# Optimization experiments

Hardware: AMD Instinct MI355X
Metric: run time of the kernel (lower is better)

The kernel has to match this reference:

```python
import jax, jax.numpy as jnp
import numpy as np

N_NODES = 50000
N_EDGES = 800000
HIDDEN = 128
N_LAYERS = 3
EPS = 1e-5


def setup_inputs() -> dict:
    key = jax.random.key(0)
    ks = jax.random.split(key, 6)
    x = jax.random.normal(ks[0], (N_NODES, HIDDEN), dtype=jnp.float32)
    edge_index = jax.random.randint(ks[1], (2, N_EDGES), 0, N_NODES, dtype=jnp.int64)
    scale = 1.0 / np.sqrt(HIDDEN)
    Wl = jax.random.normal(ks[2], (N_LAYERS, HIDDEN, HIDDEN), dtype=jnp.float32) * scale
    bl = jnp.zeros((N_LAYERS, HIDDEN), dtype=jnp.float32)
    Wr = jax.random.normal(ks[3], (N_LAYERS, HIDDEN, HIDDEN), dtype=jnp.float32) * scale
    gamma = jnp.ones((N_LAYERS, HIDDEN), dtype=jnp.float32)
    beta = jnp.zeros((N_LAYERS, HIDDEN), dtype=jnp.float32)
    return {"x": x, "edge_index": edge_index, "Wl": Wl, "bl": bl,
            "Wr": Wr, "gamma": gamma, "beta": beta}


def reference(x, edge_index, Wl, bl, Wr, gamma, beta):
    # SAGEConv (mean aggr): out_i = Wl @ mean_{j in N(i)} x_j + bl + Wr @ x_i
    # followed by BatchNorm (batch stats), ReLU, residual (layers > 0).
    src, dst = edge_index[0], edge_index[1]
    N = x.shape[0]
    deg = jax.ops.segment_sum(jnp.ones((src.shape[0],), dtype=x.dtype), dst,
                              num_segments=N)
    inv_deg = (1.0 / jnp.maximum(deg, 1.0))[:, None]  # [N,1]; empty nbhd -> 0 agg
    for i in range(N_LAYERS):
        msg = x[src]                                            # [E,H] gather
        agg = jax.ops.segment_sum(msg, dst, num_segments=N) * inv_deg  # [N,H]
        h = agg @ Wl[i].T + bl[i] + x @ Wr[i].T                 # [N,H]
        mean = jnp.mean(h, axis=0)
        var = jnp.var(h, axis=0)                                # biased, as torch BN
        h = gamma[i] * (h - mean) * jax.lax.rsqrt(var + EPS) + beta[i]
        h = jax.nn.relu(h)
        x = h + x if i > 0 else h
    return x
```

## Files before the change

kernel.cpp:

```cpp
#include <hip/hip_runtime.h>

#define HH 128
#define EPS 1e-5f
#define NBMAX 256
#define SCAP 40
#define FCAP 12288

typedef __bf16 bf16x8 __attribute__((ext_vector_type(8)));
typedef float f32x4 __attribute__((ext_vector_type(4)));
typedef float f32x2 __attribute__((ext_vector_type(2)));

__device__ __forceinline__ unsigned f2bf(float f) {
    unsigned u = __builtin_bit_cast(unsigned, f);
    return (u + 0x7FFFu + ((u >> 16) & 1u)) >> 16;
}
__device__ __forceinline__ float bflo(unsigned w) { return __builtin_bit_cast(float, w << 16); }
__device__ __forceinline__ float bfhi(unsigned w) { return __builtin_bit_cast(float, w & 0xFFFF0000u); }

__device__ __forceinline__ unsigned pack_fp8x4(float f0, float f1, float f2, float f3) {
    unsigned r = 0;
    r = __builtin_amdgcn_cvt_pk_fp8_f32(f0, f1, r, false);
    r = __builtin_amdgcn_cvt_pk_fp8_f32(f2, f3, r, true);
    return r;
}

__device__ __forceinline__ void gload_lds16(const void* g, void* l) {
    __builtin_amdgcn_global_load_lds(
        (const __attribute__((address_space(1))) unsigned int*)g,
        (__attribute__((address_space(3))) unsigned int*)l,
        16, 0, 0);
}

__global__ __launch_bounds__(256) void convert_hist_kernel(
    const float* __restrict__ x, const float* __restrict__ Wl, const float* __restrict__ Wr,
    const int* __restrict__ dst,
    ushort* __restrict__ xb, unsigned* __restrict__ xq, ushort* __restrict__ Wb,
    int* __restrict__ bcnt,
    int n4, int m4, int wtotal, int E)
{
    __shared__ int h[NBMAX];
    const int t = threadIdx.x;
    h[t] = 0;
    __syncthreads();
    const int gt = blockIdx.x * 256 + t;
    const int gs = gridDim.x * 256;
    for (int e = gt; e < E; e += gs) atomicAdd(&h[dst[e] >> 8], 1);
    for (int i = gt; i < wtotal; i += gs) {
        int l = i / (HH * 256);
        int rem = i - l * (HH * 256);
        int col = rem >> 8;
        int k = rem & 255;
        float v = (k < HH) ? Wl[(size_t)l * HH * HH + col * HH + k]
                           : Wr[(size_t)l * HH * HH + col * HH + (k - HH)];
        Wb[i] = (ushort)f2bf(v);
    }
    for (int i = gt; i < m4; i += gs) {
        uint2 o = make_uint2(0u, 0u);
        unsigned q = 0u;
        if (i < n4) {
            float4 v = ((const float4*)x)[i];
            o.x = f2bf(v.x) | (f2bf(v.y) << 16);
            o.y = f2bf(v.z) | (f2bf(v.w) << 16);
            q = pack_fp8x4(v.x, v.y, v.z, v.w);
        }
        ((uint2*)xb)[i] = o;
        xq[i] = q;
    }
    __syncthreads();
    if (h[t]) atomicAdd(&bcnt[t], h[t]);
}

__global__ __launch_bounds__(256) void bucket_scan_kernel(const int* __restrict__ bcnt,
                                                          int* __restrict__ boff,
                                                          int* __restrict__ gpos, int NB, int E) {
    __shared__ int s[NBMAX];
    const int t = threadIdx.x;
    s[t] = (t < NB) ? bcnt[t] : 0;
    __syncthreads();
    for (int off = 1; off < 256; off <<= 1) {
        int u = (t >= off) ? s[t - off] : 0;
        __syncthreads();
        s[t] += u;
        __syncthreads();
    }
    int excl = (t == 0) ? 0 : s[t - 1];
    if (t < NB) { boff[t] = excl; gpos[t] = excl; }
    if (t == 0) boff[NB] = E;
}

__global__ __launch_bounds__(256) void bucket_scatter_kernel(
    const int* __restrict__ src, const int* __restrict__ dst,
    int* __restrict__ gpos, unsigned* __restrict__ packed, int E, int GRID)
{
    __shared__ unsigned q[NBMAX][SCAP];
    __shared__ int qc[NBMAX];
    const int t = threadIdx.x;
    const int b = blockIdx.x;
    qc[t] = 0;
    __syncthreads();
    const int ebeg = (int)((long)b * E / GRID);
    const int eend = (int)((long)(b + 1) * E / GRID);
    for (int base = ebeg; base < eend; base += 256) {
        int e = base + t;
        if (e < eend) {
            int d = dst[e];
            unsigned pk = ((unsigned)d << 16) | (unsigned)src[e];
            int bk = d >> 8;
            int slot = atomicAdd(&qc[bk], 1);
            if (slot < SCAP) q[bk][slot] = pk;
            else { int p = atomicAdd(&gpos[bk], 1); packed[p] = pk; }
        }
        __syncthreads();
        int c = qc[t]; if (c > SCAP) c = SCAP;
        if (c >= 32) {
            int p = atomicAdd(&gpos[t], 32);
            for (int i = 0; i < 32; ++i) packed[p + i] = q[t][i];
            for (int i = 32; i < c; ++i) q[t][i - 32] = q[t][i];
            qc[t] = c - 32;
        } else {
            qc[t] = c;
        }
        __syncthreads();
    }
    int c = qc[t]; if (c > SCAP) c = SCAP;
    if (c > 0) {
        int p = atomicAdd(&gpos[t], c);
        for (int i = 0; i < c; ++i) packed[p + i] = q[t][i];
    }
}

__global__ __launch_bounds__(256) void bucket_finalize_kernel(
    const unsigned* __restrict__ packed, const int* __restrict__ boff,
    int* __restrict__ row_ptr, float* __restrict__ invdeg,
    ushort* __restrict__ edge_csr, int N, int E)
{
    __shared__ int hist[256];
    __shared__ int posq[256];
    __shared__ ushort outq[FCAP];
    const int b = blockIdx.x, t = threadIdx.x;
    const int beg = boff[b], end = boff[b + 1], n = end - beg;
    hist[t] = 0;
    __syncthreads();
    for (int i = beg + t; i < end; i += 256)
        atomicAdd(&hist[(packed[i] >> 16) & 255], 1);
    __syncthreads();
    const int c = hist[t];
    for (int off = 1; off < 256; off <<= 1) {
        int u = (t >= off) ? hist[t - off] : 0;
        __syncthreads();
        hist[t] += u;
        __syncthreads();
    }
    const int excl = hist[t] - c;
    const int node = (b << 8) + t;
    if (node < N) {
        row_ptr[node] = beg + excl;
        invdeg[node] = 1.0f / fmaxf((float)c, 1.0f);
    }
    if (b == 0 && t == 0) row_ptr[N] = E;
    posq[t] = excl;
    __syncthreads();
    if (n <= FCAP) {
        for (int i = beg + t; i < end; i += 256) {
            unsigned pk = packed[i];
            int p = atomicAdd(&posq[(pk >> 16) & 255], 1);
            outq[p] = (ushort)(pk & 0xFFFFu);
        }
        __syncthreads();
        for (int i = t; i < n; i += 256) edge_csr[beg + i] = outq[i];
    } else {
        for (int i = beg + t; i < end; i += 256) {
            unsigned pk = packed[i];
            int p = atomicAdd(&posq[(pk >> 16) & 255], 1);
            edge_csr[beg + p] = (ushort)(pk & 0xFFFFu);
        }
    }
}

__global__ __launch_bounds__(256) void gather_kernel(
    const unsigned* __restrict__ xq, const int* __restrict__ row_ptr,
    const ushort* __restrict__ edge_csr, const float* __restrict__ invdeg,
    ushort* __restrict__ aggb, int N)
{
    const int node = blockIdx.x * 16 + (threadIdx.x >> 4);
    const int l16 = threadIdx.x & 15;
    float a0=0,a1=0,a2=0,a3=0,a4=0,a5=0,a6=0,a7=0;
    float id = 0.f;
    if (node < N) {
        const int beg = row_ptr[node], end = row_ptr[node + 1];
        id = invdeg[node];
        int e = beg;
        for (; e + 3 < end; e += 4) {
            int s0 = edge_csr[e], s1 = edge_csr[e + 1];
            int s2 = edge_csr[e + 2], s3 = edge_csr[e + 3];
            uint2 v0 = *(const uint2*)(xq + (size_t)s0 * 32 + l16 * 2);
            uint2 v1 = *(const uint2*)(xq + (size_t)s1 * 32 + l16 * 2);
            uint2 v2 = *(const uint2*)(xq + (size_t)s2 * 32 + l16 * 2);
            uint2 v3 = *(const uint2*)(xq + (size_t)s3 * 32 + l16 * 2);
            f32x2 p;
            p = __builtin_amdgcn_cvt_pk_f32_fp8(v0.x, false); a0 += p.x; a1 += p.y;
            p = __builtin_amdgcn_cvt_pk_f32_fp8(v0.x, true);  a2 += p.x; a3 += p.y;
            p = __builtin_amdgcn_cvt_pk_f32_fp8(v0.y, false); a4 += p.x; a5 += p.y;
            p = __builtin_amdgcn_cvt_pk_f32_fp8(v0.y, true);  a6 += p.x; a7 += p.y;
            p = __builtin_amdgcn_cvt_pk_f32_fp8(v1.x, false); a0 += p.x; a1 += p.y;
            p = __builtin_amdgcn_cvt_pk_f32_fp8(v1.x, true);  a2 += p.x; a3 += p.y;
            p = __builtin_amdgcn_cvt_pk_f32_fp8(v1.y, false); a4 += p.x; a5 += p.y;
            p = __builtin_amdgcn_cvt_pk_f32_fp8(v1.y, true);  a6 += p.x; a7 += p.y;
            p = __builtin_amdgcn_cvt_pk_f32_fp8(v2.x, false); a0 += p.x; a1 += p.y;
            p = __builtin_amdgcn_cvt_pk_f32_fp8(v2.x, true);  a2 += p.x; a3 += p.y;
            p = __builtin_amdgcn_cvt_pk_f32_fp8(v2.y, false); a4 += p.x; a5 += p.y;
            p = __builtin_amdgcn_cvt_pk_f32_fp8(v2.y, true);  a6 += p.x; a7 += p.y;
            p = __builtin_amdgcn_cvt_pk_f32_fp8(v3.x, false); a0 += p.x; a1 += p.y;
            p = __builtin_amdgcn_cvt_pk_f32_fp8(v3.x, true);  a2 += p.x; a3 += p.y;
            p = __builtin_amdgcn_cvt_pk_f32_fp8(v3.y, false); a4 += p.x; a5 += p.y;
            p = __builtin_amdgcn_cvt_pk_f32_fp8(v3.y, true);  a6 += p.x; a7 += p.y;
        }
        for (; e < end; ++e) {
            int s0 = edge_csr[e];
            uint2 v0 = *(const uint2*)(xq + (size_t)s0 * 32 + l16 * 2);
            f32x2 p;
            p = __builtin_amdgcn_cvt_pk_f32_fp8(v0.x, false); a0 += p.x; a1 += p.y;
            p = __builtin_amdgcn_cvt_pk_f32_fp8(v0.x, true);  a2 += p.x; a3 += p.y;
            p = __builtin_amdgcn_cvt_pk_f32_fp8(v0.y, false); a4 += p.x; a5 += p.y;
            p = __builtin_amdgcn_cvt_pk_f32_fp8(v0.y, true);  a6 += p.x; a7 += p.y;
        }
    }
    uint4 o;
    o.x = f2bf(a0 * id) | (f2bf(a1 * id) << 16);
    o.y = f2bf(a2 * id) | (f2bf(a3 * id) << 16);
    o.z = f2bf(a4 * id) | (f2bf(a5 * id) << 16);
    o.w = f2bf(a6 * id) | (f2bf(a7 * id) << 16);
    *(uint4*)(aggb + (size_t)node * HH + l16 * 8) = o;
}

__global__ __launch_bounds__(512) void fused_layer_kernel(
    const ushort* __restrict__ aggb, ushort* __restrict__ xb,
    const ushort* __restrict__ Wb, const float* __restrict__ bl,
    const float* __restrict__ gamma, const float* __restrict__ beta,
    float* __restrict__ stats, unsigned* __restrict__ bar,
    unsigned* __restrict__ xq, float* __restrict__ outf,
    float invN, int nblocks, int N, int residual, int final_layer)
{
    extern __shared__ ushort As[];
    __shared__ float s_sum[128];
    __shared__ float s_sum2[128];

    const int tid = threadIdx.x;
    const int lane = tid & 63;
    const int wave = tid >> 6;
    const int m0 = blockIdx.x * 256;
    const int l15 = lane & 15;
    const int lg = lane >> 4;
    const int col = wave * 16 + l15;

#pragma unroll
    for (int i = 0; i < 16; ++i) {
        const int cb = (i * 8 + wave) * 64;
        const int L = cb + lane;
        const int r = L >> 5;
        const int c = L & 31;
        const int cs = (c & 0x18) | ((c & 7) ^ (r & 7));
        const ushort* gsrc = (cs < 16)
            ? (aggb + (size_t)(m0 + r) * HH + cs * 8)
            : (xb   + (size_t)(m0 + r) * HH + (cs - 16) * 8);
        gload_lds16(gsrc, &As[(size_t)cb * 8]);
    }

    bf16x8 bfr[8];
#pragma unroll
    for (int s = 0; s < 8; ++s)
        bfr[s] = *(const bf16x8*)(Wb + (size_t)col * 256 + s * 32 + lg * 8);

    if (tid < 128) { s_sum[tid] = 0.f; s_sum2[tid] = 0.f; }

    f32x4 acc[16];
#pragma unroll
    for (int rt = 0; rt < 16; ++rt) acc[rt] = (f32x4){0.f, 0.f, 0.f, 0.f};

    __syncthreads();

#pragma unroll
    for (int s = 0; s < 8; ++s) {
#pragma unroll
        for (int rt = 0; rt < 16; ++rt) {
            const int r = rt * 16 + l15;
            const int g = s * 4 + lg;
            const int c = (g & 0x18) | ((g & 7) ^ (r & 7));
            bf16x8 a = *(const bf16x8*)&As[r * 256 + c * 8];
            acc[rt] = __builtin_amdgcn_mfma_f32_16x16x32_bf16(a, bfr[s], acc[rt], 0, 0, 0);
        }
    }

    const float bias = bl[col];
    float s1 = 0.f, s2 = 0.f;
#pragma unroll
    for (int rt = 0; rt < 16; ++rt) {
#pragma unroll
        for (int r = 0; r < 4; ++r) {
            const int row = rt * 16 + lg * 4 + r;
            if (m0 + row < N) {
                float v = acc[rt][r] + bias;
                s1 += v; s2 += v * v;
            }
        }
    }
    atomicAdd(&s_sum[col], s1);
    atomicAdd(&s_sum2[col], s2);
    __syncthreads();
    if (tid < 128) {
        atomicAdd(&stats[tid], s_sum[tid]);
        atomicAdd(&stats[128 + tid], s_sum2[tid]);
    }
    __syncthreads();
    if (tid == 0) {
        __hip_atomic_fetch_add(bar, 1u, __ATOMIC_ACQ_REL, __HIP_MEMORY_SCOPE_AGENT);
        while (__hip_atomic_load(bar, __ATOMIC_ACQUIRE, __HIP_MEMORY_SCOPE_AGENT) < (unsigned)nblocks)
            __builtin_amdgcn_s_sleep(8);
    }
    __syncthreads();

    const float sA = __hip_atomic_load(&stats[col], __ATOMIC_RELAXED, __HIP_MEMORY_SCOPE_AGENT);
    const float sB = __hip_atomic_load(&stats[128 + col], __ATOMIC_RELAXED, __HIP_MEMORY_SCOPE_AGENT);
    const float mean = sA * invN;
    const float var = sB * invN - mean * mean;
    const float aa = gamma[col] * rsqrtf(var + EPS);
    const float bb = beta[col] - mean * aa;

    ushort* Cs = As;
#pragma unroll
    for (int rt = 0; rt < 16; ++rt) {
#pragma unroll
        for (int r = 0; r < 4; ++r) {
            const int row = rt * 16 + lg * 4 + r;
            float v = acc[rt][r] + bias;
            float o = fmaxf(fmaf(v, aa, bb), 0.f);
            Cs[row * 136 + col] = (ushort)f2bf(o);
        }
    }
    __syncthreads();

#pragma unroll
    for (int i = 0; i < 8; ++i) {
        const int ch = tid + i * 512;
        const int row = ch >> 4;
        const int q = ch & 15;
        const int grow = m0 + row;
        if (grow < N) {
            uint4 v = *(const uint4*)&Cs[row * 136 + q * 8];
            float o0 = bflo(v.x), o1 = bfhi(v.x);
            float o2 = bflo(v.y), o3 = bfhi(v.y);
            float o4 = bflo(v.z), o5 = bfhi(v.z);
            float o6 = bflo(v.w), o7 = bfhi(v.w);
            if (residual) {
                uint4 xw = *(const uint4*)(xb + (size_t)grow * HH + q * 8);
                o0 += bflo(xw.x); o1 += bfhi(xw.x);
                o2 += bflo(xw.y); o3 += bfhi(xw.y);
                o4 += bflo(xw.z); o5 += bfhi(xw.z);
                o6 += bflo(xw.w); o7 += bfhi(xw.w);
            }
            if (final_layer) {
                float* op = outf + (size_t)grow * HH + q * 8;
                *(float4*)op = make_float4(o0, o1, o2, o3);
                *(float4*)(op + 4) = make_float4(o4, o5, o6, o7);
            } else {
                uint4 ob;
                ob.x = f2bf(o0) | (f2bf(o1) << 16);
                ob.y = f2bf(o2) | (f2bf(o3) << 16);
                ob.z = f2bf(o4) | (f2bf(o5) << 16);
                ob.w = f2bf(o6) | (f2bf(o7) << 16);
                *(uint4*)(xb + (size_t)grow * HH + q * 8) = ob;
                uint2 qb;
                qb.x = pack_fp8x4(o0, o1, o2, o3);
                qb.y = pack_fp8x4(o4, o5, o6, o7);
                *(uint2*)(xq + (size_t)grow * 32 + q * 2) = qb;
            }
        }
    }
}

extern "C" void kernel_launch(void* const* d_in, const int* in_sizes, int n_in,
                              void* d_out, int out_size, void* d_ws, size_t ws_size,
                              hipStream_t stream) {
    const float* x     = (const float*)d_in[0];
    const int*   ei    = (const int*)d_in[1];
    const float* Wl    = (const float*)d_in[2];
    const float* bl    = (const float*)d_in[3];
    const float* Wr    = (const float*)d_in[4];
    const float* gamma = (const float*)d_in[5];
    const float* beta  = (const float*)d_in[6];
    float* out = (float*)d_out;

    const int N = in_sizes[0] / HH;
    const int E = in_sizes[1] / 2;
    const int MP = ((N + 255) / 256) * 256;
    const int NB = (N + 255) >> 8;
    const int* src = ei;
    const int* dst = ei + E;

    char* p = (char*)d_ws;
    ushort* aggb    = (ushort*)p; p += (size_t)MP * HH * 2;
    ushort* xb      = (ushort*)p; p += (size_t)MP * HH * 2;
    unsigned* xq    = (unsigned*)p; p += (size_t)MP * 32 * 4;
    ushort* Wb      = (ushort*)p; p += (size_t)3 * HH * 256 * 2;
    float* invdeg   = (float*)p;  p += (size_t)N * 4;
    char* zbase     = p;
    int* bcnt       = (int*)p;    p += NBMAX * 4;
    float* stats3   = (float*)p;  p += 768 * 4;
    unsigned* bar   = (unsigned*)p; p += 16 * 4;
    size_t zbytes   = (size_t)(p - zbase);
    int* row_ptr    = (int*)p;    p += (size_t)(N + 4) * 4;
    int* boff       = (int*)p;    p += (NBMAX + 1) * 4;
    int* gpos       = (int*)p;    p += NBMAX * 4;
    unsigned* packed = (unsigned*)p; p += (size_t)E * 4;
    ushort* edge_csr = (ushort*)p;  p += (size_t)((E + 7) & ~7) * 2;

    hipFuncSetAttribute((const void*)fused_layer_kernel,
                        hipFuncAttributeMaxDynamicSharedMemorySize, 131072);

    const int wtotal = 3 * HH * 256;
    const int n4 = N * (HH / 4);
    const int m4 = MP * (HH / 4);

    hipMemsetAsync(zbase, 0, zbytes, stream);
    convert_hist_kernel<<<1024, 256, 0, stream>>>(
        x, Wl, Wr, dst, xb, xq, Wb, bcnt, n4, m4, wtotal, E);
    bucket_scan_kernel<<<1, 256, 0, stream>>>(bcnt, boff, gpos, NB, E);
    bucket_scatter_kernel<<<256, 256, 0, stream>>>(src, dst, gpos, packed, E, 256);
    bucket_finalize_kernel<<<NB, 256, 0, stream>>>(packed, boff, row_ptr, invdeg, edge_csr, N, E);

    const int gather_blocks = MP / 16;
    const int fused_blocks = MP / 256;

    for (int layer = 0; layer < 3; ++layer) {
        gather_kernel<<<gather_blocks, 256, 0, stream>>>(
            xq, row_ptr, edge_csr, invdeg, aggb, N);

        fused_layer_kernel<<<fused_blocks, 512, 131072, stream>>>(
            aggb, xb, Wb + (size_t)layer * HH * 256, bl + (size_t)layer * HH,
            gamma + (size_t)layer * HH, beta + (size_t)layer * HH,
            stats3 + layer * 256, bar + 3 + layer,
            xq, out, 1.0f / (float)N, fused_blocks, N,
            layer > 0 ? 1 : 0, layer == 2 ? 1 : 0);
    }
}
```

Measured before the change: 213.0 us.

## Sort nodes by degree so gather warps process similar-degree nodes together

Builds a degree histogram in the finalize kernel, adds a scan and a counting-sort placement kernel that writes a node permutation, and makes the gather kernel process nodes in degree order. This is meant to cut load imbalance and divergence among the 16-lane groups in a wavefront that handle different nodes. It costs two extra small launches and an extra indirection. It also loses locality between consecutive node writes to aggb and between row_ptr reads. Padded nodes beyond N are included in the permutation, with degree 0 taken from finalize threads.

```diff
diff --git a/kernel.cpp b/kernel.cpp
--- a/kernel.cpp
+++ b/kernel.cpp
@@ -5,6 +5,7 @@
 #define NBMAX 256
 #define SCAP 40
 #define FCAP 12288
+#define DMAX 64
 
 typedef __bf16 bf16x8 __attribute__((ext_vector_type(8)));
 typedef float f32x4 __attribute__((ext_vector_type(4)));
@@ -132,7 +133,8 @@
 __global__ __launch_bounds__(256) void bucket_finalize_kernel(
     const unsigned* __restrict__ packed, const int* __restrict__ boff,
     int* __restrict__ row_ptr, float* __restrict__ invdeg,
-    ushort* __restrict__ edge_csr, int N, int E)
+    ushort* __restrict__ edge_csr, unsigned char* __restrict__ deg8,
+    int* __restrict__ dh, int N, int E)
 {
     __shared__ int hist[256];
     __shared__ int posq[256];
@@ -158,6 +160,11 @@
         invdeg[node] = 1.0f / fmaxf((float)c, 1.0f);
     }
     if (b == 0 && t == 0) row_ptr[N] = E;
+    {
+        int d = c < (DMAX - 1) ? c : (DMAX - 1);
+        deg8[node] = (unsigned char)d;
+        atomicAdd(&dh[d], 1);
+    }
     posq[t] = excl;
     __syncthreads();
     if (n <= FCAP) {
@@ -177,12 +184,38 @@
     }
 }
 
+__global__ __launch_bounds__(64) void deg_scan_kernel(const int* __restrict__ dh,
+                                                      int* __restrict__ dpos) {
+    __shared__ int s[DMAX];
+    const int t = threadIdx.x;
+    s[t] = dh[t];
+    __syncthreads();
+    for (int off = 1; off < DMAX; off <<= 1) {
+        int u = (t >= off) ? s[t - off] : 0;
+        __syncthreads();
+        s[t] += u;
+        __syncthreads();
+    }
+    dpos[t] = (t == 0) ? 0 : s[t - 1];
+}
+
+__global__ __launch_bounds__(256) void deg_place_kernel(const unsigned char* __restrict__ deg8,
+                                                        int* __restrict__ dpos,
+                                                        ushort* __restrict__ nperm, int MP) {
+    int i = blockIdx.x * 256 + threadIdx.x;
+    if (i >= MP) return;
+    int p = atomicAdd(&dpos[deg8[i]], 1);
+    nperm[p] = (ushort)i;
+}
+
 __global__ __launch_bounds__(256) void gather_kernel(
     const unsigned* __restrict__ xq, const int* __restrict__ row_ptr,
     const ushort* __restrict__ edge_csr, const float* __restrict__ invdeg,
+    const ushort* __restrict__ nperm,
     ushort* __restrict__ aggb, int N)
 {
-    const int node = blockIdx.x * 16 + (threadIdx.x >> 4);
+    const int slot = blockIdx.x * 16 + (threadIdx.x >> 4);
+    const int node = nperm[slot];
     const int l16 = threadIdx.x & 15;
     float a0=0,a1=0,a2=0,a3=0,a4=0,a5=0,a6=0,a7=0;
     float id = 0.f;
@@ -407,10 +440,14 @@
     int* bcnt       = (int*)p;    p += NBMAX * 4;
     float* stats3   = (float*)p;  p += 768 * 4;
     unsigned* bar   = (unsigned*)p; p += 16 * 4;
+    int* dh         = (int*)p;    p += DMAX * 4;
     size_t zbytes   = (size_t)(p - zbase);
+    int* dpos       = (int*)p;    p += DMAX * 4;
     int* row_ptr    = (int*)p;    p += (size_t)(N + 4) * 4;
     int* boff       = (int*)p;    p += (NBMAX + 1) * 4;
     int* gpos       = (int*)p;    p += NBMAX * 4;
+    unsigned char* deg8 = (unsigned char*)p; p += (size_t)((MP + 7) & ~7);
+    ushort* nperm   = (ushort*)p; p += (size_t)((MP + 7) & ~7) * 2;
     unsigned* packed = (unsigned*)p; p += (size_t)E * 4;
     ushort* edge_csr = (ushort*)p;  p += (size_t)((E + 7) & ~7) * 2;
 
@@ -426,14 +463,17 @@
         x, Wl, Wr, dst, xb, xq, Wb, bcnt, n4, m4, wtotal, E);
     bucket_scan_kernel<<<1, 256, 0, stream>>>(bcnt, boff, gpos, NB, E);
     bucket_scatter_kernel<<<256, 256, 0, stream>>>(src, dst, gpos, packed, E, 256);
-    bucket_finalize_kernel<<<NB, 256, 0, stream>>>(packed, boff, row_ptr, invdeg, edge_csr, N, E);
+    bucket_finalize_kernel<<<NB, 256, 0, stream>>>(packed, boff, row_ptr, invdeg,
+                                                   edge_csr, deg8, dh, N, E);
+    deg_scan_kernel<<<1, DMAX, 0, stream>>>(dh, dpos);
+    deg_place_kernel<<<(MP + 255) / 256, 256, 0, stream>>>(deg8, dpos, nperm, MP);
 
     const int gather_blocks = MP / 16;
     const int fused_blocks = MP / 256;
 
     for (int layer = 0; layer < 3; ++layer) {
         gather_kernel<<<gather_blocks, 256, 0, stream>>>(
-            xq, row_ptr, edge_csr, invdeg, aggb, N);
+            xq, row_ptr, edge_csr, invdeg, nperm, aggb, N);
 
         fused_layer_kernel<<<fused_blocks, 512, 131072, stream>>>(
             aggb, xb, Wb + (size_t)layer * HH * 256, bl + (size_t)layer * HH,
```

Result: slower. 475.5 us (+123.2%).
